# Kernel tuning notes

Measured on AMD Instinct MI355X. Metric: run time of the kernel, lower is better.

The kernel has to match this reference:

```python
import jax, jax.numpy as jnp
import numpy as np

NG, N, NFG, NFR, NFP, B = 4, 64, 1024, 256, 256, 2048
SCALE = 1.0 / float(np.sqrt(NFR + NFP))
EPS = 1e-5  # torch LayerNorm default


def setup_inputs() -> dict:
    key = jax.random.key(0)
    k = jax.random.split(key, 4)
    x = jax.random.normal(k[0], (B, N, NFG), dtype=jnp.float32)
    # per-graph params stacked over NG for vectorized computation
    Wt = jax.random.normal(k[1], (NG, NFR, NFG), dtype=jnp.float32) * 0.02
    bt = jnp.zeros((NG, NFR), dtype=jnp.float32)
    Wp = jax.random.normal(k[2], (NG, NFR, NFG), dtype=jnp.float32) * 0.02
    bp = jnp.zeros((NG, NFR), dtype=jnp.float32)
    Wg = jax.random.normal(k[3], (NG, NFG, NFG), dtype=jnp.float32) * 0.02  # [out,in]
    gamma = jnp.ones((NG, NFG), dtype=jnp.float32)
    beta = jnp.zeros((NG, NFG), dtype=jnp.float32)
    return {"x": x, "Wt": Wt, "bt": bt, "Wp": Wp, "bp": bp,
            "Wg": Wg, "gamma": gamma, "beta": beta}


def reference(x, Wt, bt, Wp, bp, Wg, gamma, beta):
    # theta/phi projections, vectorized over NG graphs: [G,B,N,R]
    theta = jnp.einsum('bnf,grf->gbnr', x, Wt) + bt[:, None, None, :]
    phi = jnp.einsum('bnf,grf->gbnr', x, Wp) + bp[:, None, None, :]
    # original computes sim=theta@phi^T then .sum(2); identical math:
    # relation[b,n] = theta[b,n] . sum_m phi[b,m]  (avoids the NxN matrix)
    phi_sum = phi.sum(axis=2)                                  # [G,B,R]
    relation = jnp.einsum('gbnr,gbr->gbn', theta, phi_sum) * SCALE
    w = jax.nn.softmax(relation, axis=2)                       # softmax over boxes N
    # attention-weighted aggregation over boxes -> [G,B,NFG]
    agg = jnp.einsum('gbn,bnf->gbf', w, x)
    # GCN linear (no bias): [G,B,NFG]
    h = jnp.einsum('gbf,gof->gbo', agg, Wg)
    # LayerNorm over feature dim, per graph
    mu = h.mean(axis=-1, keepdims=True)
    var = ((h - mu) ** 2).mean(axis=-1, keepdims=True)
    h = (h - mu) * jax.lax.rsqrt(var + EPS) * gamma[:, None, :] + beta[:, None, :]
    h = jax.nn.relu(h)
    # mean over the NG graphs; restore keepdim axis -> [B,1,NFG]
    return h.mean(axis=0)[:, None, :]
```

## Files before the change

kernel.cpp:

```cpp
#include <hip/hip_runtime.h>
#include <hip/hip_bf16.h>

typedef __attribute__((ext_vector_type(4))) float f4;
typedef __attribute__((ext_vector_type(4))) float f32x4;
typedef __attribute__((ext_vector_type(8))) short short8;
typedef __attribute__((ext_vector_type(2))) unsigned int u32x2;
typedef __attribute__((ext_vector_type(4))) unsigned int u32x4;
typedef unsigned int u32;
typedef unsigned short u16;

#define SCALE_F 0.04419417382415922f

__device__ inline u16 f2bf(float f) {
  u32 u = __float_as_uint(f);
  u32 r = u + 0x7FFFu + ((u >> 16) & 1u);
  return (u16)(r >> 16);
}
__device__ inline float bflo(u32 u) { return __uint_as_float(u << 16); }
__device__ inline float bfhi(u32 u) { return __uint_as_float(u & 0xFFFF0000u); }

#define GLD16(gsrc, ldst)                                                     \
  __builtin_amdgcn_global_load_lds(                                           \
      (const __attribute__((address_space(1))) void*)(gsrc),                  \
      (__attribute__((address_space(3))) void*)(ldst), 16, 0, 0)

__device__ __forceinline__ void cvt8(const float* __restrict__ src,
                                     u16* __restrict__ dst, int blk, int t) {
  int i = blk * 256 + t;
  const f4* s = (const f4*)src;
  f4 a = s[(size_t)i * 2];
  f4 b = s[(size_t)i * 2 + 1];
  u32x4 p;
  p[0] = (u32)f2bf(a[0]) | ((u32)f2bf(a[1]) << 16);
  p[1] = (u32)f2bf(a[2]) | ((u32)f2bf(a[3]) << 16);
  p[2] = (u32)f2bf(b[0]) | ((u32)f2bf(b[1]) << 16);
  p[3] = (u32)f2bf(b[2]) | ((u32)f2bf(b[3]) << 16);
  *(u32x4*)(dst + (size_t)i * 8) = p;
}

__global__ __launch_bounds__(256) void k0_prep(const float* __restrict__ Wg,
                                               const float* __restrict__ Wp,
                                               const float* __restrict__ Wt,
                                               u16* __restrict__ wgb,
                                               u16* __restrict__ wpb,
                                               u16* __restrict__ wtb) {
  const int blk = blockIdx.x, t = threadIdx.x;
  if (blk < 2048) {
    cvt8(Wg, wgb, blk, t);
  } else if (blk < 2560) {
    cvt8(Wp, wpb, blk - 2048, t);
  } else {
    __shared__ u16 tile[64][66];
    const int bid = blk - 2560;
    const int g = bid >> 6, rem = bid & 63;
    const int f0 = (rem & 15) * 64, r0 = (rem >> 4) * 64;
    const float* src = Wt + ((size_t)g * 256 + r0) * 1024 + f0;
#pragma unroll
    for (int i = 0; i < 16; ++i) {
      int idx = t + i * 256;
      int rl = idx >> 6, fl = idx & 63;
      tile[fl][rl] = f2bf(src[rl * 1024 + fl]);
    }
    __syncthreads();
    u16* dst = wtb + ((size_t)g * 1024 + f0) * 256 + r0;
#pragma unroll
    for (int i = 0; i < 4; ++i) {
      int idx = t + i * 256;
      int fl = idx >> 4, rq = idx & 15;
      u32x2 p;
      p[0] = (u32)tile[fl][rq * 4]     | ((u32)tile[fl][rq * 4 + 1] << 16);
      p[1] = (u32)tile[fl][rq * 4 + 2] | ((u32)tile[fl][rq * 4 + 3] << 16);
      *(u32x2*)(dst + fl * 256 + rq * 4) = p;
    }
  }
}

__global__ __launch_bounds__(256) void k1_prep(const float* __restrict__ x,
                                               u16* __restrict__ xs16,
                                               char* __restrict__ xpre) {
  const int b = blockIdx.x, t = threadIdx.x;
  const float* xb = x + (size_t)b * 65536;
  char* xp = xpre + (size_t)b * 131072;
  const int slot = t >> 1, half = t & 1;
  f4 acc = {0.f, 0.f, 0.f, 0.f};
#pragma unroll 8
  for (int n = 0; n < 64; ++n) {
    f4 v = *(const f4*)(xb + n * 1024 + t * 4);
    acc += v;
    u32 p0 = (u32)f2bf(v[0]) | ((u32)f2bf(v[1]) << 16);
    u32 p1 = (u32)f2bf(v[2]) | ((u32)f2bf(v[3]) << 16);
    char* dst = xp + n * 2048 + ((slot ^ (n & 7)) << 4) + half * 8;
    ((u32*)dst)[0] = p0;
    ((u32*)dst)[1] = p1;
  }
  u32x2 p;
  p[0] = (u32)f2bf(acc[0]) | ((u32)f2bf(acc[1]) << 16);
  p[1] = (u32)f2bf(acc[2]) | ((u32)f2bf(acc[3]) << 16);
  *(u32x2*)(xs16 + (size_t)b * 1024 + t * 4) = p;
}

__global__ __launch_bounds__(256) void k2_gemm(const u16* __restrict__ A,
                                               const u16* __restrict__ Bt,
                                               const float* __restrict__ bp,
                                               u16* __restrict__ C) {
  const int n0 = blockIdx.x * 64, m0 = blockIdx.y * 128;
  __shared__ u16 Al[128 * 32];
  __shared__ u16 Bl[64 * 32];
  const int t = threadIdx.x;
  const int w = t >> 6, l = t & 63;
  const int lr = l & 15, lh = l >> 4;
  f32x4 acc[2][4] = {};
  for (int kt = 0; kt < 1024; kt += 32) {
#pragma unroll
    for (int j = 0; j < 2; ++j) {
      int idx = t + j * 256;
      int row = idx >> 2, sl = idx & 3;
      GLD16(A + (size_t)(m0 + row) * 1024 + kt + sl * 8, Al + idx * 8);
    }
    {
      int row = t >> 2, sl = t & 3;
      GLD16(Bt + (size_t)(n0 + row) * 1024 + kt + sl * 8, Bl + t * 8);
    }
    __syncthreads();
    short8 af[2], bfr[4];
#pragma unroll
    for (int m = 0; m < 2; ++m)
      af[m] = *(const short8*)(Al + (w * 32 + m * 16 + lr) * 32 + lh * 8);
#pragma unroll
    for (int n = 0; n < 4; ++n)
      bfr[n] = *(const short8*)(Bl + (n * 16 + lr) * 32 + lh * 8);
#pragma unroll
    for (int m = 0; m < 2; ++m)
#pragma unroll
      for (int n = 0; n < 4; ++n)
        acc[m][n] = __builtin_amdgcn_mfma_f32_16x16x32_bf16(af[m], bfr[n],
                                                            acc[m][n], 0, 0, 0);
    __syncthreads();
  }
#pragma unroll
  for (int m = 0; m < 2; ++m)
#pragma unroll
    for (int n = 0; n < 4; ++n) {
      int col = n0 + n * 16 + lr;
      float bb = 64.0f * bp[col];
#pragma unroll
      for (int j = 0; j < 4; ++j)
        C[(size_t)(m0 + w * 32 + m * 16 + lh * 4 + j) * 1024 + col] =
            f2bf(acc[m][n][j] + bb);
    }
}

__global__ __launch_bounds__(256) void k3_gemm(const u16* __restrict__ A,
                                               const u16* __restrict__ Btt,
                                               u16* __restrict__ Vb) {
  const int g = blockIdx.z;
  const int n0 = blockIdx.x * 128, m0 = blockIdx.y * 128;
  const u16* Bg = Btt + (size_t)g * 1024 * 256;
  __shared__ u16 Al[128 * 32];
  __shared__ u16 Bl[128 * 32];
  const int t = threadIdx.x;
  const int w = t >> 6, l = t & 63;
  const int wr = w >> 1, wc = w & 1;
  const int lr = l & 15, lh = l >> 4;
  f32x4 acc[4][4] = {};
  for (int kt = 0; kt < 256; kt += 32) {
#pragma unroll
    for (int j = 0; j < 2; ++j) {
      int idx = t + j * 256;
      int row = idx >> 2, sl = idx & 3;
      GLD16(A + (size_t)(m0 + row) * 1024 + g * 256 + kt + sl * 8, Al + idx * 8);
      GLD16(Bg + (size_t)(n0 + row) * 256 + kt + sl * 8, Bl + idx * 8);
    }
    __syncthreads();
    short8 af[4], bfr[4];
#pragma unroll
    for (int m = 0; m < 4; ++m)
      af[m] = *(const short8*)(Al + (wr * 64 + m * 16 + lr) * 32 + lh * 8);
#pragma unroll
    for (int n = 0; n < 4; ++n)
      bfr[n] = *(const short8*)(Bl + (wc * 64 + n * 16 + lr) * 32 + lh * 8);
#pragma unroll
    for (int m = 0; m < 4; ++m)
#pragma unroll
      for (int n = 0; n < 4; ++n)
        acc[m][n] = __builtin_amdgcn_mfma_f32_16x16x32_bf16(af[m], bfr[n],
                                                            acc[m][n], 0, 0, 0);
    __syncthreads();
  }
  u16* Vg = Vb + (size_t)g * 2048 * 1024;
#pragma unroll
  for (int m = 0; m < 4; ++m)
#pragma unroll
    for (int n = 0; n < 4; ++n)
#pragma unroll
      for (int j = 0; j < 4; ++j)
        Vg[(size_t)(m0 + wr * 64 + m * 16 + lh * 4 + j) * 1024 +
           (n0 + wc * 64 + n * 16 + lr)] = f2bf(acc[m][n][j]);
}

__device__ __forceinline__ void relation_phase(const char* xl, const u16* vb,
                                               float* relp, int w, int l) {
  const int lg = l >> 4, lr = l & 15;
  f32x4 racc[4] = {};
#pragma unroll
  for (int kp = 0; kp < 2; ++kp) {
    const int kt = kp * 512 + w * 32;
    short8 afr = {};
    if (lr < 4) afr = *(const short8*)(vb + lr * 1032 + kt + lg * 8);
#pragma unroll
    for (int nt = 0; nt < 4; ++nt) {
      int n = nt * 16 + lr;
      short8 bfrg = *(const short8*)(
          xl + n * 2048 + ((((kt >> 3) + lg) ^ (n & 7)) << 4));
      racc[nt] = __builtin_amdgcn_mfma_f32_16x16x32_bf16(afr, bfrg, racc[nt],
                                                         0, 0, 0);
    }
  }
  if (l < 16) {
#pragma unroll
    for (int nt = 0; nt < 4; ++nt)
#pragma unroll
      for (int j = 0; j < 4; ++j)
        relp[(w * 4 + j) * 64 + nt * 16 + lr] = racc[nt][j];
  }
}

__device__ __forceinline__ void softmax_phase(const float* relp, float* wsm,
                                              int t) {
  if (t < 256) {
    const int g = t >> 6, n = t & 63;
    float rel = 0.f;
#pragma unroll
    for (int ww = 0; ww < 16; ++ww) rel += relp[(ww * 4 + g) * 64 + n];
    rel *= SCALE_F;
    float mx = rel;
#pragma unroll
    for (int o = 32; o > 0; o >>= 1) mx = fmaxf(mx, __shfl_xor(mx, o, 64));
    float e = __expf(rel - mx);
    float s = e;
#pragma unroll
    for (int o = 32; o > 0; o >>= 1) s += __shfl_xor(s, o, 64);
    wsm[t] = e / s;
  }
}

__device__ __forceinline__ void agg_phase(const char* xl, const float* wsm,
                                          float* relp, u16* aggb, int b,
                                          int t) {
  const int hh = t >> 9, r = t & 511, g = r >> 7, f8 = r & 127;
  const float* wg = wsm + g * 64 + hh * 32;
  float a0 = 0, a1 = 0, a2 = 0, a3 = 0, a4 = 0, a5 = 0, a6 = 0, a7 = 0;
#pragma unroll 8
  for (int n0 = 0; n0 < 32; ++n0) {
    int n = hh * 32 + n0;
    float wv = wg[n0];
    u32x4 xp = *(const u32x4*)(xl + n * 2048 + ((f8 ^ (n & 7)) << 4));
    a0 = fmaf(bflo(xp[0]), wv, a0);
    a1 = fmaf(bfhi(xp[0]), wv, a1);
    a2 = fmaf(bflo(xp[1]), wv, a2);
    a3 = fmaf(bfhi(xp[1]), wv, a3);
    a4 = fmaf(bflo(xp[2]), wv, a4);
    a5 = fmaf(bfhi(xp[2]), wv, a5);
    a6 = fmaf(bflo(xp[3]), wv, a6);
    a7 = fmaf(bfhi(xp[3]), wv, a7);
  }
  if (hh) {
    f4 q0 = {a0, a1, a2, a3};
    f4 q1 = {a4, a5, a6, a7};
    *(f4*)(relp + r * 8) = q0;
    *(f4*)(relp + r * 8 + 4) = q1;
  }
  __syncthreads();
  if (!hh) {
    f4 q0 = *(const f4*)(relp + r * 8);
    f4 q1 = *(const f4*)(relp + r * 8 + 4);
    u32x4 p;
    p[0] = (u32)f2bf(a0 + q0[0]) | ((u32)f2bf(a1 + q0[1]) << 16);
    p[1] = (u32)f2bf(a2 + q0[2]) | ((u32)f2bf(a3 + q0[3]) << 16);
    p[2] = (u32)f2bf(a4 + q1[0]) | ((u32)f2bf(a5 + q1[1]) << 16);
    p[3] = (u32)f2bf(a6 + q1[2]) | ((u32)f2bf(a7 + q1[3]) << 16);
    *(u32x4*)(aggb + ((size_t)g * 2048 + b) * 1024 + f8 * 8) = p;
  }
}

#define K4_LDS (131072 + 8256 + 16384 + 1024)
__global__ __launch_bounds__(1024) void k4_fused(const char* __restrict__ xpre,
                                                 const u16* __restrict__ vb16,
                                                 u16* __restrict__ aggb) {
  extern __shared__ char sm[];
  char* xl = sm;
  u16* vb = (u16*)(sm + 131072);
  float* relp = (float*)(sm + 131072 + 8256);
  float* wsm = (float*)(sm + 131072 + 8256 + 16384);
  const int t = threadIdx.x;
  const int w = t >> 6, l = t & 63;
  const int b0 = (1023 - blockIdx.x) * 2, b1 = b0 + 1;

  {
    int g = t >> 8, q = t & 255;
    u32x2 pv = *(const u32x2*)(vb16 + ((size_t)g * 2048 + b0) * 1024 + q * 4);
    *(u32x2*)(vb + g * 1032 + q * 4) = pv;
  }
  const char* xg0 = xpre + (size_t)b0 * 131072;
#pragma unroll
  for (int i = 0; i < 8; ++i)
    GLD16(xg0 + (w * 8 + i) * 1024 + l * 16, xl + (w * 8 + i) * 1024 + l * 16);
  __syncthreads();

  const char* xg1 = xpre + (size_t)b1 * 131072;
  u32x4 pf0 = *(const u32x4*)(xg1 + t * 16);
  u32x4 pf1 = *(const u32x4*)(xg1 + t * 16 + 16384);
  u32x4 pf2 = *(const u32x4*)(xg1 + t * 16 + 32768);
  u32x4 pf3 = *(const u32x4*)(xg1 + t * 16 + 49152);
  u32x4 pf4 = *(const u32x4*)(xg1 + t * 16 + 65536);
  u32x4 pf5 = *(const u32x4*)(xg1 + t * 16 + 81920);
  u32x4 pf6 = *(const u32x4*)(xg1 + t * 16 + 98304);
  u32x4 pf7 = *(const u32x4*)(xg1 + t * 16 + 114688);
  u32x2 pv1 =
      *(const u32x2*)(vb16 + ((size_t)(t >> 8) * 2048 + b1) * 1024 + (t & 255) * 4);

  relation_phase(xl, vb, relp, w, l);
  __syncthreads();
  softmax_phase(relp, wsm, t);
  __syncthreads();
  agg_phase(xl, wsm, relp, aggb, b0, t);
  __syncthreads();

  *(u32x4*)(xl + t * 16) = pf0;
  *(u32x4*)(xl + t * 16 + 16384) = pf1;
  *(u32x4*)(xl + t * 16 + 32768) = pf2;
  *(u32x4*)(xl + t * 16 + 49152) = pf3;
  *(u32x4*)(xl + t * 16 + 65536) = pf4;
  *(u32x4*)(xl + t * 16 + 81920) = pf5;
  *(u32x4*)(xl + t * 16 + 98304) = pf6;
  *(u32x4*)(xl + t * 16 + 114688) = pf7;
  {
    int g = t >> 8, q = t & 255;
    *(u32x2*)(vb + g * 1032 + q * 4) = pv1;
  }
  __syncthreads();

  relation_phase(xl, vb, relp, w, l);
  __syncthreads();
  softmax_phase(relp, wsm, t);
  __syncthreads();
  agg_phase(xl, wsm, relp, aggb, b1, t);
}

__global__ __launch_bounds__(256) void k5_gemm(const u16* __restrict__ Ab,
                                               const u16* __restrict__ Bb,
                                               u16* __restrict__ H) {
  const int g = blockIdx.z;
  const int n0 = blockIdx.x * 128, m0 = blockIdx.y * 128;
  const u16* A = Ab + (size_t)g * 2048 * 1024;
  const u16* Bt = Bb + (size_t)g * 1024 * 1024;
  __shared__ u16 Al[128 * 32];
  __shared__ u16 Bl[128 * 32];
  const int t = threadIdx.x;
  const int w = t >> 6, l = t & 63;
  const int wr = w >> 1, wc = w & 1;
  const int lr = l & 15, lh = l >> 4;
  f32x4 acc[4][4] = {};
  for (int kt = 0; kt < 1024; kt += 32) {
#pragma unroll
    for (int j = 0; j < 2; ++j) {
      int idx = t + j * 256;
      int row = idx >> 2, sl = idx & 3;
      GLD16(A + (size_t)(m0 + row) * 1024 + kt + sl * 8, Al + idx * 8);
      GLD16(Bt + (size_t)(n0 + row) * 1024 + kt + sl * 8, Bl + idx * 8);
    }
    __syncthreads();
    short8 af[4], bfr[4];
#pragma unroll
    for (int m = 0; m < 4; ++m)
      af[m] = *(const short8*)(Al + (wr * 64 + m * 16 + lr) * 32 + lh * 8);
#pragma unroll
    for (int n = 0; n < 4; ++n)
      bfr[n] = *(const short8*)(Bl + (wc * 64 + n * 16 + lr) * 32 + lh * 8);
#pragma unroll
    for (int m = 0; m < 4; ++m)
#pragma unroll
      for (int n = 0; n < 4; ++n)
        acc[m][n] = __builtin_amdgcn_mfma_f32_16x16x32_bf16(af[m], bfr[n],
                                                            acc[m][n], 0, 0, 0);
    __syncthreads();
  }
  u16* Hg = H + (size_t)g * 2048 * 1024;
#pragma unroll
  for (int m = 0; m < 4; ++m)
#pragma unroll
    for (int n = 0; n < 4; ++n)
#pragma unroll
      for (int j = 0; j < 4; ++j)
        Hg[(size_t)(m0 + wr * 64 + m * 16 + lh * 4 + j) * 1024 +
           (n0 + wc * 64 + n * 16 + lr)] = f2bf(acc[m][n][j]);
}

__global__ __launch_bounds__(256) void k6_ln(const u16* __restrict__ H,
                                             const float* __restrict__ gamma,
                                             const float* __restrict__ beta,
                                             float* __restrict__ out) {
  const int b = blockIdx.x, t = threadIdx.x;
  const int w = t >> 6, lane = t & 63;
  __shared__ float red[8];
  f4 acc = {0.f, 0.f, 0.f, 0.f};
  for (int g = 0; g < 4; ++g) {
    u32x2 hp = *(const u32x2*)(H + ((size_t)g * 2048 + b) * 1024 + t * 4);
    f4 hv = {bflo(hp[0]), bfhi(hp[0]), bflo(hp[1]), bfhi(hp[1])};
    float s = hv[0] + hv[1] + hv[2] + hv[3];
    float q = hv[0] * hv[0] + hv[1] * hv[1] + hv[2] * hv[2] + hv[3] * hv[3];
#pragma unroll
    for (int o = 32; o > 0; o >>= 1) {
      s += __shfl_xor(s, o, 64);
      q += __shfl_xor(q, o, 64);
    }
    if (lane == 0) { red[w] = s; red[4 + w] = q; }
    __syncthreads();
    s = red[0] + red[1] + red[2] + red[3];
    q = red[4] + red[5] + red[6] + red[7];
    float mean = s * (1.f / 1024.f);
    float var = q * (1.f / 1024.f) - mean * mean;
    float rstd = rsqrtf(var + 1e-5f);
    f4 gm = *(const f4*)(gamma + g * 1024 + t * 4);
    f4 bt = *(const f4*)(beta + g * 1024 + t * 4);
#pragma unroll
    for (int j = 0; j < 4; ++j) {
      float val = (hv[j] - mean) * rstd * gm[j] + bt[j];
      acc[j] += fmaxf(val, 0.f);
    }
    __syncthreads();
  }
  acc *= 0.25f;
  *(f4*)(out + (size_t)b * 1024 + t * 4) = acc;
}

extern "C" void kernel_launch(void* const* d_in, const int* in_sizes, int n_in,
                              void* d_out, int out_size, void* d_ws, size_t ws_size,
                              hipStream_t stream) {
  const float* x     = (const float*)d_in[0];
  const float* Wt    = (const float*)d_in[1];
  const float* Wp    = (const float*)d_in[3];
  const float* bp    = (const float*)d_in[4];
  const float* Wg    = (const float*)d_in[5];
  const float* gamma = (const float*)d_in[6];
  const float* beta  = (const float*)d_in[7];
  float* out = (float*)d_out;

  char* ws = (char*)d_ws;
  u16*   xs16 = (u16*)(ws);
  u16*   ps16 = (u16*)(ws + (4u << 20));
  u16*   wpb  = (u16*)(ws + (8u << 20));
  u16*   wtb  = (u16*)(ws + (10u << 20));
  u16*   wgb  = (u16*)(ws + (12u << 20));
  u16*   vb16 = (u16*)(ws + (20u << 20));
  u16*   aggb = (u16*)(ws + (36u << 20));
  u16*   hb16 = (u16*)(ws + (52u << 20));
  char*  xpre = (char*)(ws + (68u << 20));

  hipFuncSetAttribute((const void*)k4_fused,
                      hipFuncAttributeMaxDynamicSharedMemorySize, K4_LDS);

  k0_prep<<<2816, 256, 0, stream>>>(Wg, Wp, Wt, wgb, wpb, wtb);
  k1_prep<<<2048, 256, 0, stream>>>(x, xs16, xpre);
  k2_gemm<<<dim3(16, 16), 256, 0, stream>>>(xs16, wpb, bp, ps16);
  k3_gemm<<<dim3(8, 16, 4), 256, 0, stream>>>(ps16, wtb, vb16);
  k4_fused<<<1024, 1024, K4_LDS, stream>>>(xpre, vb16, aggb);
  k5_gemm<<<dim3(8, 16, 4), 256, 0, stream>>>(aggb, wgb, hb16);
  k6_ln<<<2048, 256, 0, stream>>>(hb16, gamma, beta, out);
}
```

Baseline: 336.1 us.

## Merge x and weight prep kernels; move xpre swizzle to the k4 load side

Combines the weight-conversion and x-conversion prep kernels into one launch, so the x blocks and weight blocks share a grid and one launch gap is removed. The x prep now writes 16-byte contiguous bf16 chunks linearly, with each thread covering 8 features over half the rows and a shared-memory reduction for the column sums. The XOR swizzle that used to be applied when writing xpre is now applied to the global addresses in k4's global-to-LDS and prefetch loads, so the LDS layout stays the same. This trades narrower scattered stores for wider coalesced ones, at the cost of an extra LDS reduction and a barrier in the prep blocks.

```diff
diff --git a/kernel.cpp b/kernel.cpp
--- a/kernel.cpp
+++ b/kernel.cpp
@@ -16,6 +16,9 @@
   u32 r = u + 0x7FFFu + ((u >> 16) & 1u);
   return (u16)(r >> 16);
 }
+__device__ inline u32 pk(float a, float b) {
+  return (u32)f2bf(a) | ((u32)f2bf(b) << 16);
+}
 __device__ inline float bflo(u32 u) { return __uint_as_float(u << 16); }
 __device__ inline float bfhi(u32 u) { return __uint_as_float(u & 0xFFFF0000u); }
 
@@ -23,6 +26,8 @@
   __builtin_amdgcn_global_load_lds(                                           \
       (const __attribute__((address_space(1))) void*)(gsrc),                  \
       (__attribute__((address_space(3))) void*)(ldst), 16, 0, 0)
+
+#define SWZ(o) (((o) & ~2047) | (((((o) >> 4) & 127) ^ (((o) >> 11) & 7)) << 4))
 
 __device__ __forceinline__ void cvt8(const float* __restrict__ src,
                                      u16* __restrict__ dst, int blk, int t) {
@@ -31,27 +36,69 @@
   f4 a = s[(size_t)i * 2];
   f4 b = s[(size_t)i * 2 + 1];
   u32x4 p;
-  p[0] = (u32)f2bf(a[0]) | ((u32)f2bf(a[1]) << 16);
-  p[1] = (u32)f2bf(a[2]) | ((u32)f2bf(a[3]) << 16);
-  p[2] = (u32)f2bf(b[0]) | ((u32)f2bf(b[1]) << 16);
-  p[3] = (u32)f2bf(b[2]) | ((u32)f2bf(b[3]) << 16);
+  p[0] = pk(a[0], a[1]);
+  p[1] = pk(a[2], a[3]);
+  p[2] = pk(b[0], b[1]);
+  p[3] = pk(b[2], b[3]);
   *(u32x4*)(dst + (size_t)i * 8) = p;
 }
 
-__global__ __launch_bounds__(256) void k0_prep(const float* __restrict__ Wg,
-                                               const float* __restrict__ Wp,
-                                               const float* __restrict__ Wt,
-                                               u16* __restrict__ wgb,
-                                               u16* __restrict__ wpb,
-                                               u16* __restrict__ wtb) {
+__global__ __launch_bounds__(256) void k01_prep(const float* __restrict__ x,
+                                                const float* __restrict__ Wg,
+                                                const float* __restrict__ Wp,
+                                                const float* __restrict__ Wt,
+                                                u16* __restrict__ xs16,
+                                                char* __restrict__ xpre,
+                                                u16* __restrict__ wgb,
+                                                u16* __restrict__ wpb,
+                                                u16* __restrict__ wtb) {
+  __shared__ float red[256][8];
+  __shared__ u16 tile[64][66];
   const int blk = blockIdx.x, t = threadIdx.x;
   if (blk < 2048) {
-    cvt8(Wg, wgb, blk, t);
-  } else if (blk < 2560) {
-    cvt8(Wp, wpb, blk - 2048, t);
+    const int b = blk;
+    const float* xb = x + (size_t)b * 65536;
+    char* xp = xpre + (size_t)b * 131072;
+    const int g16 = t & 127, rp = t >> 7;
+    f4 acc0 = {0.f, 0.f, 0.f, 0.f}, acc1 = {0.f, 0.f, 0.f, 0.f};
+#pragma unroll 8
+    for (int it = 0; it < 32; ++it) {
+      int n = it * 2 + rp;
+      const float* src = xb + n * 1024 + g16 * 8;
+      f4 v0 = *(const f4*)(src);
+      f4 v1 = *(const f4*)(src + 4);
+      acc0 += v0;
+      acc1 += v1;
+      u32x4 p;
+      p[0] = pk(v0[0], v0[1]);
+      p[1] = pk(v0[2], v0[3]);
+      p[2] = pk(v1[0], v1[1]);
+      p[3] = pk(v1[2], v1[3]);
+      *(u32x4*)(xp + n * 2048 + g16 * 16) = p;
+    }
+    *(f4*)&red[t][0] = acc0;
+    *(f4*)&red[t][4] = acc1;
+    __syncthreads();
+    if (t < 128) {
+      f4 s0 = *(const f4*)&red[t][0];
+      f4 s1 = *(const f4*)&red[t][4];
+      f4 q0 = *(const f4*)&red[t + 128][0];
+      f4 q1 = *(const f4*)&red[t + 128][4];
+      s0 += q0;
+      s1 += q1;
+      u32x4 p;
+      p[0] = pk(s0[0], s0[1]);
+      p[1] = pk(s0[2], s0[3]);
+      p[2] = pk(s1[0], s1[1]);
+      p[3] = pk(s1[2], s1[3]);
+      *(u32x4*)(xs16 + (size_t)b * 1024 + t * 8) = p;
+    }
+  } else if (blk < 4096) {
+    cvt8(Wg, wgb, blk - 2048, t);
+  } else if (blk < 4608) {
+    cvt8(Wp, wpb, blk - 4096, t);
   } else {
-    __shared__ u16 tile[64][66];
-    const int bid = blk - 2560;
+    const int bid = blk - 4608;
     const int g = bid >> 6, rem = bid & 63;
     const int f0 = (rem & 15) * 64, r0 = (rem >> 4) * 64;
     const float* src = Wt + ((size_t)g * 256 + r0) * 1024 + f0;
@@ -73,30 +120,6 @@
       *(u32x2*)(dst + fl * 256 + rq * 4) = p;
     }
   }
-}
-
-__global__ __launch_bounds__(256) void k1_prep(const float* __restrict__ x,
-                                               u16* __restrict__ xs16,
-                                               char* __restrict__ xpre) {
-  const int b = blockIdx.x, t = threadIdx.x;
-  const float* xb = x + (size_t)b * 65536;
-  char* xp = xpre + (size_t)b * 131072;
-  const int slot = t >> 1, half = t & 1;
-  f4 acc = {0.f, 0.f, 0.f, 0.f};
-#pragma unroll 8
-  for (int n = 0; n < 64; ++n) {
-    f4 v = *(const f4*)(xb + n * 1024 + t * 4);
-    acc += v;
-    u32 p0 = (u32)f2bf(v[0]) | ((u32)f2bf(v[1]) << 16);
-    u32 p1 = (u32)f2bf(v[2]) | ((u32)f2bf(v[3]) << 16);
-    char* dst = xp + n * 2048 + ((slot ^ (n & 7)) << 4) + half * 8;
-    ((u32*)dst)[0] = p0;
-    ((u32*)dst)[1] = p1;
-  }
-  u32x2 p;
-  p[0] = (u32)f2bf(acc[0]) | ((u32)f2bf(acc[1]) << 16);
-  p[1] = (u32)f2bf(acc[2]) | ((u32)f2bf(acc[3]) << 16);
-  *(u32x2*)(xs16 + (size_t)b * 1024 + t * 4) = p;
 }
 
 __global__ __launch_bounds__(256) void k2_gemm(const u16* __restrict__ A,
@@ -275,10 +298,10 @@
     f4 q0 = *(const f4*)(relp + r * 8);
     f4 q1 = *(const f4*)(relp + r * 8 + 4);
     u32x4 p;
-    p[0] = (u32)f2bf(a0 + q0[0]) | ((u32)f2bf(a1 + q0[1]) << 16);
-    p[1] = (u32)f2bf(a2 + q0[2]) | ((u32)f2bf(a3 + q0[3]) << 16);
-    p[2] = (u32)f2bf(a4 + q1[0]) | ((u32)f2bf(a5 + q1[1]) << 16);
-    p[3] = (u32)f2bf(a6 + q1[2]) | ((u32)f2bf(a7 + q1[3]) << 16);
+    p[0] = pk(a0 + q0[0], a1 + q0[1]);
+    p[1] = pk(a2 + q0[2], a3 + q0[3]);
+    p[2] = pk(a4 + q1[0], a5 + q1[1]);
+    p[3] = pk(a6 + q1[2], a7 + q1[3]);
     *(u32x4*)(aggb + ((size_t)g * 2048 + b) * 1024 + f8 * 8) = p;
   }
 }
@@ -303,19 +326,21 @@
   }
   const char* xg0 = xpre + (size_t)b0 * 131072;
 #pragma unroll
-  for (int i = 0; i < 8; ++i)
-    GLD16(xg0 + (w * 8 + i) * 1024 + l * 16, xl + (w * 8 + i) * 1024 + l * 16);
+  for (int i = 0; i < 8; ++i) {
+    int o = (w * 8 + i) * 1024 + l * 16;
+    GLD16(xg0 + SWZ(o), xl + o);
+  }
   __syncthreads();
 
   const char* xg1 = xpre + (size_t)b1 * 131072;
-  u32x4 pf0 = *(const u32x4*)(xg1 + t * 16);
-  u32x4 pf1 = *(const u32x4*)(xg1 + t * 16 + 16384);
-  u32x4 pf2 = *(const u32x4*)(xg1 + t * 16 + 32768);
-  u32x4 pf3 = *(const u32x4*)(xg1 + t * 16 + 49152);
-  u32x4 pf4 = *(const u32x4*)(xg1 + t * 16 + 65536);
-  u32x4 pf5 = *(const u32x4*)(xg1 + t * 16 + 81920);
-  u32x4 pf6 = *(const u32x4*)(xg1 + t * 16 + 98304);
-  u32x4 pf7 = *(const u32x4*)(xg1 + t * 16 + 114688);
+  u32x4 pf0 = *(const u32x4*)(xg1 + SWZ(t * 16));
+  u32x4 pf1 = *(const u32x4*)(xg1 + SWZ(t * 16 + 16384));
+  u32x4 pf2 = *(const u32x4*)(xg1 + SWZ(t * 16 + 32768));
+  u32x4 pf3 = *(const u32x4*)(xg1 + SWZ(t * 16 + 49152));
+  u32x4 pf4 = *(const u32x4*)(xg1 + SWZ(t * 16 + 65536));
+  u32x4 pf5 = *(const u32x4*)(xg1 + SWZ(t * 16 + 81920));
+  u32x4 pf6 = *(const u32x4*)(xg1 + SWZ(t * 16 + 98304));
+  u32x4 pf7 = *(const u32x4*)(xg1 + SWZ(t * 16 + 114688));
   u32x2 pv1 =
       *(const u32x2*)(vb16 + ((size_t)(t >> 8) * 2048 + b1) * 1024 + (t & 255) * 4);
 
@@ -460,8 +485,7 @@
   hipFuncSetAttribute((const void*)k4_fused,
                       hipFuncAttributeMaxDynamicSharedMemorySize, K4_LDS);
 
-  k0_prep<<<2816, 256, 0, stream>>>(Wg, Wp, Wt, wgb, wpb, wtb);
-  k1_prep<<<2048, 256, 0, stream>>>(x, xs16, xpre);
+  k01_prep<<<4864, 256, 0, stream>>>(x, Wg, Wp, Wt, xs16, xpre, wgb, wpb, wtb);
   k2_gemm<<<dim3(16, 16), 256, 0, stream>>>(xs16, wpb, bp, ps16);
   k3_gemm<<<dim3(8, 16, 4), 256, 0, stream>>>(ps16, wtb, vb16);
   k4_fused<<<1024, 1024, K4_LDS, stream>>>(xpre, vb16, aggb);
```

Measured after the change: 329.3 us. 1.02x faster.
